# Optimization experiments

Measured on AMD Instinct MI355X. Metric: run time of the kernel, lower is better.

## Reference

```python
import jax, jax.numpy as jnp
import numpy as np
import math

N = 192
KN = 500000.0
MU = 0.5           # friction_coefficient
EPS = 1e-4         # eplis grid value
_alpha = -math.log(0.7) / math.pi
_gamma = _alpha / math.sqrt(_alpha ** 2 + 1.0)
ETA = 2.0 * _gamma * math.sqrt(KN * 1.0)  # damping_coefficient_Eta, particle_mass=1
FILTER = 5


def setup_inputs() -> dict:
    key = jax.random.key(0)
    ks = jax.random.split(key, 6)
    shape = (N, N, N)
    x_grid = jax.random.uniform(ks[0], shape, dtype=jnp.float32) * N
    y_grid = jax.random.uniform(ks[1], shape, dtype=jnp.float32) * N
    z_grid = jax.random.uniform(ks[2], shape, dtype=jnp.float32) * N
    vx_grid = jax.random.normal(ks[3], shape, dtype=jnp.float32) * 0.1
    vy_grid = jax.random.normal(ks[4], shape, dtype=jnp.float32) * 0.1
    vz_grid = jax.random.normal(ks[5], shape, dtype=jnp.float32) * 0.1
    d = jnp.float32(0.5)
    return {"x_grid": x_grid, "y_grid": y_grid, "z_grid": z_grid,
            "vx_grid": vx_grid, "vy_grid": vy_grid, "vz_grid": vz_grid, "d": d}


def _shifts():
    # Loop order in source: for i: for j: for k -> roll shifts (k-2, j-2, i-2)
    s = [(k - 2, j - 2, i - 2) for i in range(FILTER) for j in range(FILTER) for k in range(FILTER)]
    return jnp.array(s, dtype=jnp.int32)  # (125, 3)


def _dem_forces(x_grid, y_grid, z_grid, vx_grid, vy_grid, vz_grid, d):
    two_d = 2.0 * d
    zero = jnp.float32(0.0)

    def body(carry, shift):
        fxc, fyc, fzc, fxd, fyd, fzd, frx, fry, frz = carry
        roll3 = lambda g: jnp.roll(g, shift, axis=(0, 1, 2))
        diffx = x_grid - roll3(x_grid)
        diffy = y_grid - roll3(y_grid)
        diffz = z_grid - roll3(z_grid)
        dist = jnp.sqrt(diffx ** 2 + diffy ** 2 + diffz ** 2)
        overlap = dist < two_d
        safe = jnp.maximum(EPS, dist)
        # collision (accumulated)
        coef = KN * (dist - two_d) / safe
        fxc = fxc + jnp.where(overlap, coef * diffx, zero)
        fyc = fyc + jnp.where(overlap, coef * diffy, zero)
        fzc = fzc + jnp.where(overlap, coef * diffz, zero)
        # damping (accumulated)
        diffvx = vx_grid - roll3(vx_grid)
        diffvy = vy_grid - roll3(vy_grid)
        diffvz = vz_grid - roll3(vz_grid)
        diffv_Vn = (diffvx * diffx + diffvy * diffy + diffvz * diffz) / safe
        fxd = fxd + jnp.where(overlap, ETA * diffv_Vn * diffx / safe, zero)
        fyd = fyd + jnp.where(overlap, ETA * diffv_Vn * diffy / safe, zero)
        fzd = fzd + jnp.where(overlap, ETA * diffv_Vn * diffz / safe, zero)
        # friction (overwritten each offset; uses updated accumulators, incl. the
        # original source's use of diffvy in the z-friction numerator)
        frx = -jnp.where(overlap, jnp.abs(jnp.abs(MU * fyc) + jnp.abs(MU * fzc) - MU * fxd)
                         * diffvx / jnp.maximum(EPS, jnp.abs(diffvx)), zero)
        fry = -jnp.where(overlap, jnp.abs(jnp.abs(MU * fxc) + jnp.abs(MU * fzc) - MU * fyd)
                         * diffvy / jnp.maximum(EPS, jnp.abs(diffvy)), zero)
        frz = -jnp.where(overlap, jnp.abs(jnp.abs(MU * fxc) + jnp.abs(MU * fyc) - MU * fzd)
                         * diffvy / jnp.maximum(EPS, jnp.abs(diffvz)), zero)
        return (fxc, fyc, fzc, fxd, fyd, fzd, frx, fry, frz), None

    z = jnp.zeros_like(x_grid)
    init = (z, z, z, z, z, z, z, z, z)
    carry, _ = jax.lax.scan(body, init, _shifts())
    return jnp.stack(carry)  # (9, N, N, N)


def reference(x_grid, y_grid, z_grid, vx_grid, vy_grid, vz_grid, d):
    return _dem_forces(x_grid, y_grid, z_grid, vx_grid, vy_grid, vz_grid, d)
```

## Files before the change

### kernel.cpp

```cpp
#include <hip/hip_runtime.h>
#include <math.h>

#define N   192
#define NNN (N * N * N)
#define K   4
#define XB  (N / K)

__device__ __forceinline__ int wrapN(int v) {
  if (v < 0)  v += N;
  if (v >= N) v -= N;
  return v;
}

__global__ void __launch_bounds__(256)
dem_forces_k4(const float* __restrict__ xg,  const float* __restrict__ yg,
              const float* __restrict__ zg,  const float* __restrict__ vxg,
              const float* __restrict__ vyg, const float* __restrict__ vzg,
              const float* __restrict__ dp,  float* __restrict__ out)
{
  const int t  = blockIdx.x * 256 + threadIdx.x;
  const int xb = t % XB;
  const int x0 = xb * K;
  const int r  = t / XB;
  const int y  = r % N;
  const int z  = r / N;

  const float KN  = 500000.0f;
  const float EPS = 1e-4f;
  const float MU  = 0.5f;
  const double alpha_d = 0.35667494393873245 / 3.141592653589793;
  const float  ETA = (float)(2.0 * (alpha_d / sqrt(alpha_d * alpha_d + 1.0)) * sqrt(500000.0));

  const float two_d = 2.0f * dp[0];
  const float two2  = two_d * two_d;
  const float two2m = two2 * 1.000002f;

  const int cellBase = (z * N + y) * N + x0;

  const float4 xc4 = *reinterpret_cast<const float4*>(xg + cellBase);
  const float4 yc4 = *reinterpret_cast<const float4*>(yg + cellBase);
  const float4 zc4 = *reinterpret_cast<const float4*>(zg + cellBase);
  const float xcv[K] = {xc4.x, xc4.y, xc4.z, xc4.w};
  const float ycv[K] = {yc4.x, yc4.y, yc4.z, yc4.w};
  const float zcv[K] = {zc4.x, zc4.y, zc4.z, zc4.w};

  float acc[6][K];
#pragma unroll
  for (int f = 0; f < 6; ++f)
#pragma unroll
    for (int c = 0; c < K; ++c) acc[f][c] = 0.0f;

  int cs[3];
  cs[0] = x0 - 4; if (cs[0] < 0)  cs[0] += N;
  cs[1] = x0;
  cs[2] = x0 + 4; if (cs[2] >= N) cs[2] -= N;

#pragma unroll 1
  for (int a = 0; a < 5; ++a) {
    const int zz = wrapN(z + 2 - a);
#pragma unroll 1
    for (int b = 0; b < 5; ++b) {
      const int yy   = wrapN(y + 2 - b);
      const int rowb = (zz * N + yy) * N;

      float nx[12], ny[12], nz[12];
#pragma unroll
      for (int j = 0; j < 3; ++j) {
        const float4 ax = *reinterpret_cast<const float4*>(xg + rowb + cs[j]);
        const float4 ay = *reinterpret_cast<const float4*>(yg + rowb + cs[j]);
        const float4 az = *reinterpret_cast<const float4*>(zg + rowb + cs[j]);
        nx[4*j+0] = ax.x; nx[4*j+1] = ax.y; nx[4*j+2] = ax.z; nx[4*j+3] = ax.w;
        ny[4*j+0] = ay.x; ny[4*j+1] = ay.y; ny[4*j+2] = ay.z; ny[4*j+3] = ay.w;
        nz[4*j+0] = az.x; nz[4*j+1] = az.y; nz[4*j+2] = az.z; nz[4*j+3] = az.w;
      }

      float d2min = 1e30f;
#pragma unroll
      for (int c = 0; c < K; ++c) {
#pragma unroll
        for (int i = 0; i < 5; ++i) {
          const int p = c + 6 - i;
          const float dx = xcv[c] - nx[p];
          const float dy = ycv[c] - ny[p];
          const float dz = zcv[c] - nz[p];
          const float d2 = dx*dx + dy*dy + dz*dz;
          d2min = fminf(d2min, d2);
        }
      }

      if (__any(d2min < two2m)) {
#pragma unroll
        for (int c = 0; c < K; ++c) {
#pragma unroll
          for (int i = 0; i < 5; ++i) {
            const int p = c + 6 - i;
            const float dx = xcv[c] - nx[p];
            const float dy = ycv[c] - ny[p];
            const float dz = zcv[c] - nz[p];
            const float d2 = dx*dx + dy*dy + dz*dz;
            if (d2 < two2m) {
              const float dist = sqrtf(d2);
              const bool  ov   = dist < two_d;
              const float safe = fmaxf(EPS, dist);
              const float coef = KN * (dist - two_d) / safe;
              const int ci   = cellBase + c;
              const int nidx = rowb + wrapN(x0 + c + 2 - i);
              const float dvx = vxg[ci] - vxg[nidx];
              const float dvy = vyg[ci] - vyg[nidx];
              const float dvz = vzg[ci] - vzg[nidx];
              const float vn  = (dvx*dx + dvy*dy + dvz*dz) / safe;
              const float evn = ETA * vn;
              if (ov) {
                acc[0][c] += coef * dx;
                acc[1][c] += coef * dy;
                acc[2][c] += coef * dz;
                acc[3][c] += (evn * dx) / safe;
                acc[4][c] += (evn * dy) / safe;
                acc[5][c] += (evn * dz) / safe;
              }
            }
          }
        }
      }
    }
  }

  float frx[K], fry[K], frz[K];
#pragma unroll
  for (int c = 0; c < K; ++c) { frx[c] = 0.f; fry[c] = 0.f; frz[c] = 0.f; }
  {
    const int rowb = (wrapN(z - 2) * N + wrapN(y - 2)) * N;
    float d2v[K], dxv[K], dyv[K], dzv[K];
    float d2min = 1e30f;
#pragma unroll
    for (int c = 0; c < K; ++c) {
      const int nidx = rowb + wrapN(x0 + c - 2);
      const float dx = xcv[c] - xg[nidx];
      const float dy = ycv[c] - yg[nidx];
      const float dz = zcv[c] - zg[nidx];
      dxv[c] = dx; dyv[c] = dy; dzv[c] = dz;
      d2v[c] = dx*dx + dy*dy + dz*dz;
      d2min  = fminf(d2min, d2v[c]);
    }
    if (__any(d2min < two2m)) {
#pragma unroll
      for (int c = 0; c < K; ++c) {
        if (d2v[c] < two2m) {
          const float dist = sqrtf(d2v[c]);
          if (dist < two_d) {
            const int ci   = cellBase + c;
            const int nidx = rowb + wrapN(x0 + c - 2);
            const float dvx = vxg[ci] - vxg[nidx];
            const float dvy = vyg[ci] - vyg[nidx];
            const float dvz = vzg[ci] - vzg[nidx];
            frx[c] = -(fabsf(fabsf(MU*acc[1][c]) + fabsf(MU*acc[2][c]) - MU*acc[3][c])
                       * dvx / fmaxf(EPS, fabsf(dvx)));
            fry[c] = -(fabsf(fabsf(MU*acc[0][c]) + fabsf(MU*acc[2][c]) - MU*acc[4][c])
                       * dvy / fmaxf(EPS, fabsf(dvy)));
            frz[c] = -(fabsf(fabsf(MU*acc[0][c]) + fabsf(MU*acc[1][c]) - MU*acc[5][c])
                       * dvy / fmaxf(EPS, fabsf(dvz)));
          }
        }
      }
    }
  }

#pragma unroll
  for (int f = 0; f < 6; ++f) {
    float4 o; o.x = acc[f][0]; o.y = acc[f][1]; o.z = acc[f][2]; o.w = acc[f][3];
    *reinterpret_cast<float4*>(out + f * NNN + cellBase) = o;
  }
  {
    float4 o;
    o.x = frx[0]; o.y = frx[1]; o.z = frx[2]; o.w = frx[3];
    *reinterpret_cast<float4*>(out + 6 * NNN + cellBase) = o;
    o.x = fry[0]; o.y = fry[1]; o.z = fry[2]; o.w = fry[3];
    *reinterpret_cast<float4*>(out + 7 * NNN + cellBase) = o;
    o.x = frz[0]; o.y = frz[1]; o.z = frz[2]; o.w = frz[3];
    *reinterpret_cast<float4*>(out + 8 * NNN + cellBase) = o;
  }
}

extern "C" void kernel_launch(void* const* d_in, const int* in_sizes, int n_in,
                              void* d_out, int out_size, void* d_ws, size_t ws_size,
                              hipStream_t stream) {
  const float* xg  = (const float*)d_in[0];
  const float* yg  = (const float*)d_in[1];
  const float* zg  = (const float*)d_in[2];
  const float* vxg = (const float*)d_in[3];
  const float* vyg = (const float*)d_in[4];
  const float* vzg = (const float*)d_in[5];
  const float* dp  = (const float*)d_in[6];
  float* out = (float*)d_out;

  const int threads = NNN / K;
  dem_forces_k4<<<threads / 256, 256, 0, stream>>>(xg, yg, zg, vxg, vyg, vzg, dp, out);
}
```

Measured before the change: 602.8 us.

## Software-pipeline neighbor row loads and cheapen overlap pre-check with sign-bit OR

Flattens the 5x5 neighbor-row loop into one loop that prefetches the next row's x/y/z float4s into a second register buffer while computing the current row, overlapping global load latency with compute. The pre-check builds d2 minus threshold with FMAs and ORs the sign bits instead of taking a running min. For the center row it skips the self-pair, so self-overlap alone no longer triggers the slow path. Block indices are remapped in strides of 8 to spread neighboring tiles across XCDs/L2 slices. The cost is more live registers from the double buffer.

```diff
diff --git a/kernel.cpp b/kernel.cpp
--- a/kernel.cpp
+++ b/kernel.cpp
@@ -5,6 +5,7 @@
 #define NNN (N * N * N)
 #define K   4
 #define XB  (N / K)
+#define NBLK (NNN / K / 256)
 
 __device__ __forceinline__ int wrapN(int v) {
   if (v < 0)  v += N;
@@ -12,28 +13,106 @@
   return v;
 }
 
+#define ROWB(AA, BB, DST) do {                                          \
+    int zz = z + 2 - (AA); if (zz >= N) zz -= N; if (zz < 0) zz += N;   \
+    int yy = y + 2 - (BB); if (yy >= N) yy -= N; if (yy < 0) yy += N;   \
+    DST = (zz * N + yy) * N; } while (0)
+
+#define LOADROW(PX, PY, PZ, RB) do {                                    \
+    const int _o0 = (RB) + cs0, _o1 = (RB) + cs1, _o2 = (RB) + cs2;     \
+    PX[0] = *reinterpret_cast<const float4*>(xg + _o0);                 \
+    PY[0] = *reinterpret_cast<const float4*>(yg + _o0);                 \
+    PZ[0] = *reinterpret_cast<const float4*>(zg + _o0);                 \
+    PX[1] = *reinterpret_cast<const float4*>(xg + _o1);                 \
+    PY[1] = *reinterpret_cast<const float4*>(yg + _o1);                 \
+    PZ[1] = *reinterpret_cast<const float4*>(zg + _o1);                 \
+    PX[2] = *reinterpret_cast<const float4*>(xg + _o2);                 \
+    PY[2] = *reinterpret_cast<const float4*>(yg + _o2);                 \
+    PZ[2] = *reinterpret_cast<const float4*>(zg + _o2);                 \
+  } while (0)
+
+#define COMPUTE(PX, PY, PZ, ROWBV, CENTER) do {                              \
+  const float ex[8] = {PX[0].z, PX[0].w, PX[1].x, PX[1].y,                   \
+                       PX[1].z, PX[1].w, PX[2].x, PX[2].y};                  \
+  const float ey[8] = {PY[0].z, PY[0].w, PY[1].x, PY[1].y,                   \
+                       PY[1].z, PY[1].w, PY[2].x, PY[2].y};                  \
+  const float ez[8] = {PZ[0].z, PZ[0].w, PZ[1].x, PZ[1].y,                   \
+                       PZ[1].z, PZ[1].w, PZ[2].x, PZ[2].y};                  \
+  unsigned uo = 0u, us = 0u;                                                 \
+  _Pragma("unroll")                                                          \
+  for (int c = 0; c < K; ++c) {                                              \
+    _Pragma("unroll")                                                        \
+    for (int i = 0; i < 5; ++i) {                                            \
+      const int p = c + 4 - i;                                               \
+      const float dx = xcv[c] - ex[p];                                       \
+      const float dy = ycv[c] - ey[p];                                       \
+      const float dz = zcv[c] - ez[p];                                       \
+      const float tv = fmaf(dz, dz, fmaf(dy, dy, fmaf(dx, dx, negT)));       \
+      if (i == 2) us |= __float_as_uint(tv);                                 \
+      else        uo |= __float_as_uint(tv);                                 \
+    }                                                                        \
+  }                                                                          \
+  const unsigned ug = (CENTER) ? uo : (uo | us);                             \
+  if (__any((int)ug < 0)) {                                                  \
+    _Pragma("unroll")                                                        \
+    for (int c = 0; c < K; ++c) {                                            \
+      _Pragma("unroll")                                                      \
+      for (int i = 0; i < 5; ++i) {                                          \
+        if ((CENTER) && i == 2) continue;                                    \
+        const int p = c + 4 - i;                                             \
+        const float dx = xcv[c] - ex[p];                                     \
+        const float dy = ycv[c] - ey[p];                                     \
+        const float dz = zcv[c] - ez[p];                                     \
+        const float d2 = dx*dx + dy*dy + dz*dz;                              \
+        if (d2 < two2m) {                                                    \
+          const float dist = sqrtf(d2);                                      \
+          const bool  ov   = dist < two_d;          \
+          const float safe = fmaxf(EPS, dist);                               \
+          const float coef = KN * (dist - two_d) / safe;                     \
+          const int ci   = cellBase + c;                                     \
+          const int nidx = (ROWBV) + wrapN(x0 + c + 2 - i);                  \
+          const float dvx = vxg[ci] - vxg[nidx];                             \
+          const float dvy = vyg[ci] - vyg[nidx];                             \
+          const float dvz = vzg[ci] - vzg[nidx];                             \
+          const float vn  = (dvx*dx + dvy*dy + dvz*dz) / safe;               \
+          const float evn = ETA * vn;                                        \
+          if (ov) {                                                          \
+            acc[0][c] += coef * dx;                                          \
+            acc[1][c] += coef * dy;                                          \
+            acc[2][c] += coef * dz;                                          \
+            acc[3][c] += (evn * dx) / safe;                                  \
+            acc[4][c] += (evn * dy) / safe;                                  \
+            acc[5][c] += (evn * dz) / safe;                                  \
+          }                                                                  \
+        }                                                                    \
+      }                                                                      \
+    }                                                                        \
+  }                                                                          \
+} while (0)
+
 __global__ void __launch_bounds__(256)
-dem_forces_k4(const float* __restrict__ xg,  const float* __restrict__ yg,
-              const float* __restrict__ zg,  const float* __restrict__ vxg,
-              const float* __restrict__ vyg, const float* __restrict__ vzg,
-              const float* __restrict__ dp,  float* __restrict__ out)
+dem_forces_k4p(const float* __restrict__ xg,  const float* __restrict__ yg,
+               const float* __restrict__ zg,  const float* __restrict__ vxg,
+               const float* __restrict__ vyg, const float* __restrict__ vzg,
+               const float* __restrict__ dp,  float* __restrict__ out)
 {
-  const int t  = blockIdx.x * 256 + threadIdx.x;
-  const int xb = t % XB;
-  const int x0 = xb * K;
-  const int r  = t / XB;
-  const int y  = r % N;
-  const int z  = r / N;
+  const int bid  = (int)(blockIdx.x % 8u) * (NBLK / 8) + (int)(blockIdx.x / 8u);
+  const int t    = bid * 256 + threadIdx.x;
+  const int xb   = t % XB;
+  const int x0   = xb * K;
+  const int r    = t / XB;
+  const int y    = r % N;
+  const int z    = r / N;
 
   const float KN  = 500000.0f;
   const float EPS = 1e-4f;
   const float MU  = 0.5f;
   const double alpha_d = 0.35667494393873245 / 3.141592653589793;
-  const float  ETA = (float)(2.0 * (alpha_d / sqrt(alpha_d * alpha_d + 1.0)) * sqrt(500000.0));
+  const float  ETA = (float)(2.0 * (alpha_d / sqrt(alpha_d*alpha_d + 1.0)) * sqrt(500000.0));
 
   const float two_d = 2.0f * dp[0];
-  const float two2  = two_d * two_d;
-  const float two2m = two2 * 1.000002f;
+  const float two2m = (two_d * two_d) * 1.000002f;
+  const float negT  = -two2m;
 
   const int cellBase = (z * N + y) * N + x0;
 
@@ -50,80 +129,32 @@
 #pragma unroll
     for (int c = 0; c < K; ++c) acc[f][c] = 0.0f;
 
-  int cs[3];
-  cs[0] = x0 - 4; if (cs[0] < 0)  cs[0] += N;
-  cs[1] = x0;
-  cs[2] = x0 + 4; if (cs[2] >= N) cs[2] -= N;
-
+  int cs0 = x0 - 4; if (cs0 < 0) cs0 += N;
+  const int cs1 = x0;
+  int cs2 = x0 + 4; if (cs2 >= N) cs2 -= N;
+
+  float4 Ax[3], Ay[3], Az[3], Bx[3], By[3], Bz[3];
+
+  int rb0, rb1;
+  ROWB(0, 0, rb0);
+  LOADROW(Ax, Ay, Az, rb0);
+
+  int a = 0, b = 0;
 #pragma unroll 1
-  for (int a = 0; a < 5; ++a) {
-    const int zz = wrapN(z + 2 - a);
-#pragma unroll 1
-    for (int b = 0; b < 5; ++b) {
-      const int yy   = wrapN(y + 2 - b);
-      const int rowb = (zz * N + yy) * N;
-
-      float nx[12], ny[12], nz[12];
-#pragma unroll
-      for (int j = 0; j < 3; ++j) {
-        const float4 ax = *reinterpret_cast<const float4*>(xg + rowb + cs[j]);
-        const float4 ay = *reinterpret_cast<const float4*>(yg + rowb + cs[j]);
-        const float4 az = *reinterpret_cast<const float4*>(zg + rowb + cs[j]);
-        nx[4*j+0] = ax.x; nx[4*j+1] = ax.y; nx[4*j+2] = ax.z; nx[4*j+3] = ax.w;
-        ny[4*j+0] = ay.x; ny[4*j+1] = ay.y; ny[4*j+2] = ay.z; ny[4*j+3] = ay.w;
-        nz[4*j+0] = az.x; nz[4*j+1] = az.y; nz[4*j+2] = az.z; nz[4*j+3] = az.w;
-      }
-
-      float d2min = 1e30f;
-#pragma unroll
-      for (int c = 0; c < K; ++c) {
-#pragma unroll
-        for (int i = 0; i < 5; ++i) {
-          const int p = c + 6 - i;
-          const float dx = xcv[c] - nx[p];
-          const float dy = ycv[c] - ny[p];
-          const float dz = zcv[c] - nz[p];
-          const float d2 = dx*dx + dy*dy + dz*dz;
-          d2min = fminf(d2min, d2);
-        }
-      }
-
-      if (__any(d2min < two2m)) {
-#pragma unroll
-        for (int c = 0; c < K; ++c) {
-#pragma unroll
-          for (int i = 0; i < 5; ++i) {
-            const int p = c + 6 - i;
-            const float dx = xcv[c] - nx[p];
-            const float dy = ycv[c] - ny[p];
-            const float dz = zcv[c] - nz[p];
-            const float d2 = dx*dx + dy*dy + dz*dz;
-            if (d2 < two2m) {
-              const float dist = sqrtf(d2);
-              const bool  ov   = dist < two_d;
-              const float safe = fmaxf(EPS, dist);
-              const float coef = KN * (dist - two_d) / safe;
-              const int ci   = cellBase + c;
-              const int nidx = rowb + wrapN(x0 + c + 2 - i);
-              const float dvx = vxg[ci] - vxg[nidx];
-              const float dvy = vyg[ci] - vyg[nidx];
-              const float dvz = vzg[ci] - vzg[nidx];
-              const float vn  = (dvx*dx + dvy*dy + dvz*dz) / safe;
-              const float evn = ETA * vn;
-              if (ov) {
-                acc[0][c] += coef * dx;
-                acc[1][c] += coef * dy;
-                acc[2][c] += coef * dz;
-                acc[3][c] += (evn * dx) / safe;
-                acc[4][c] += (evn * dy) / safe;
-                acc[5][c] += (evn * dz) / safe;
-              }
-            }
-          }
-        }
-      }
-    }
-  }
+  for (int rr = 0; rr < 24; rr += 2) {
+    int a1 = a, b1 = b + 1; if (b1 == 5) { b1 = 0; ++a1; }
+    ROWB(a1, b1, rb1);
+    LOADROW(Bx, By, Bz, rb1);
+    COMPUTE(Ax, Ay, Az, rb0, (rr == 12));
+
+    int a2 = a1, b2 = b1 + 1; if (b2 == 5) { b2 = 0; ++a2; }
+    int rb2; ROWB(a2, b2, rb2);
+    LOADROW(Ax, Ay, Az, rb2);
+    COMPUTE(Bx, By, Bz, rb1, false);
+
+    rb0 = rb2; a = a2; b = b2;
+  }
+  COMPUTE(Ax, Ay, Az, rb0, false);
 
   float frx[K], fry[K], frz[K];
 #pragma unroll
@@ -193,6 +224,5 @@
   const float* dp  = (const float*)d_in[6];
   float* out = (float*)d_out;
 
-  const int threads = NNN / K;
-  dem_forces_k4<<<threads / 256, 256, 0, stream>>>(xg, yg, zg, vxg, vyg, vzg, dp, out);
+  dem_forces_k4p<<<NBLK, 256, 0, stream>>>(xg, yg, zg, vxg, vyg, vzg, dp, out);
 }
```

After: 547.7 us. -9.1%, faster.
